# Kernel optimization log

Measured on AMD Instinct MI355X. Metric: run time of the kernel, lower is better.

The kernel has to match this reference:

```python
import jax, jax.numpy as jnp
import numpy as np

N, E, G = 20000, 320000, 64
DIN, H, EF, FC, OUT = 128, 256, 16, 256, 1
BN_EPS = 1e-5


def _gine_layer(x, src, dst, edge_attr, We, be, Wa, ba, g, bt, Wb, bb):
    # GINEConv (eps=0): out = mlp(x + sum_j relu(x_j + lin_edge(e_ij)))
    e = edge_attr @ We.T + be                      # [E, in_ch]
    m = jax.nn.relu(x[src] + e)                    # messages [E, in_ch]
    agg = jax.ops.segment_sum(m, dst, num_segments=x.shape[0])
    h = (x + agg) @ Wa.T + ba                      # Linear
    # BatchNorm1d in eval mode with running_mean=0, running_var=1
    inv = jax.lax.rsqrt(jnp.asarray(1.0 + BN_EPS, h.dtype))
    h = jax.nn.relu(h * inv * g + bt)
    return jax.nn.relu(h @ Wb.T + bb)


def _mean_pool(h, batch, num_graphs):
    sums = jax.ops.segment_sum(h, batch, num_segments=num_graphs)
    cnt = jax.ops.segment_sum(jnp.ones((h.shape[0],), h.dtype), batch, num_segments=num_graphs)
    return sums / jnp.maximum(cnt, 1.0)[:, None]


def setup_inputs() -> dict:
    key = jax.random.key(0)
    ks = iter(jax.random.split(key, 64))

    def nrm(shape, s=0.05):
        return jax.random.normal(next(ks), shape, jnp.float32) * s

    inp = {
        "x": jax.random.normal(next(ks), (N, DIN), jnp.float32),
        "edge_attr": jax.random.normal(next(ks), (E, EF), jnp.float32),
        "src": jax.random.randint(next(ks), (E,), 0, N),
        "dst": jax.random.randint(next(ks), (E,), 0, N),
        "batch": jnp.sort(jax.random.randint(next(ks), (N,), 0, G)),
    }
    dims = [(DIN, H), (H, H), (H, H)]
    for i, (din, h) in enumerate(dims, start=1):
        inp[f"We{i}"] = nrm((din, EF));  inp[f"be{i}"] = jnp.zeros((din,), jnp.float32)
        inp[f"Wa{i}"] = nrm((h, din));  inp[f"ba{i}"] = jnp.zeros((h,), jnp.float32)
        inp[f"g{i}"] = jnp.ones((h,), jnp.float32); inp[f"bt{i}"] = jnp.zeros((h,), jnp.float32)
        inp[f"Wb{i}"] = nrm((h, h));    inp[f"bb{i}"] = jnp.zeros((h,), jnp.float32)
    inp["L1w"] = nrm((FC * 3, H * 3)); inp["L1b"] = jnp.zeros((FC * 3,), jnp.float32)
    inp["L2w"] = nrm((OUT, FC * 3));   inp["L2b"] = jnp.zeros((OUT,), jnp.float32)
    return inp


def reference(x, edge_attr, src, dst, batch,
              We1, be1, Wa1, ba1, g1, bt1, Wb1, bb1,
              We2, be2, Wa2, ba2, g2, bt2, Wb2, bb2,
              We3, be3, Wa3, ba3, g3, bt3, Wb3, bb3,
              L1w, L1b, L2w, L2b):
    h1 = _gine_layer(x,  src, dst, edge_attr, We1, be1, Wa1, ba1, g1, bt1, Wb1, bb1)
    h2 = _gine_layer(h1, src, dst, edge_attr, We2, be2, Wa2, ba2, g2, bt2, Wb2, bb2)
    h3 = _gine_layer(h2, src, dst, edge_attr, We3, be3, Wa3, ba3, g3, bt3, Wb3, bb3)
    p = jnp.concatenate([_mean_pool(h1, batch, G),
                         _mean_pool(h2, batch, G),
                         _mean_pool(h3, batch, G)], axis=1)   # [G, 3H]
    h = jax.nn.relu(p @ L1w.T + L1b)   # dropout is identity (training=False)
    return jax.nn.sigmoid(h @ L2w.T + L2b)
```

## Files before the change

### kernel.cpp

```cpp
#include <hip/hip_runtime.h>
#include <math.h>
#include <stdint.h>

#define N_NODES 20000
#define M_PAD 20032
#define N_EDGES 320000
#define N_GRAPHS 64
#define DIN 128
#define H 256
#define POOL_W 768
#define CHUNK 40
#define NCHUNK (N_EDGES / CHUNK)

typedef __attribute__((ext_vector_type(8))) short bf16x8;
typedef __attribute__((ext_vector_type(4))) float f32x4;
typedef __attribute__((ext_vector_type(4))) unsigned int u32x4;
typedef __attribute__((ext_vector_type(2))) unsigned int u32x2;
typedef _Float16 h2 __attribute__((ext_vector_type(2)));

__device__ __forceinline__ unsigned short f2bf(float f) {
    unsigned u = __builtin_bit_cast(unsigned, f);
    u += 0x7FFFu + ((u >> 16) & 1u);
    return (unsigned short)(u >> 16);
}
__device__ __forceinline__ float bf2f(unsigned short u) {
    return __builtin_bit_cast(float, (unsigned)u << 16);
}
__device__ __forceinline__ unsigned short f2h(float f) {
    const _Float16 h = (_Float16)f;
    return __builtin_bit_cast(unsigned short, h);
}

#if __has_builtin(__builtin_amdgcn_fdot2)
#define DOT2(a, b, c) __builtin_amdgcn_fdot2((a), (b), (c), false)
#else
__device__ __forceinline__ float dot2_fallback(h2 a, h2 b, float c) {
    return fmaf((float)a.x, (float)b.x, fmaf((float)a.y, (float)b.y, c));
}
#define DOT2(a, b, c) dot2_fallback((a), (b), (c))
#endif

struct CvtJob  { const float* s; unsigned short* d; int n4; int mode; int kdim; };
struct CvtJobs { CvtJob j[12]; };

__global__ __launch_bounds__(256) void cvt_all(CvtJobs jobs)
{
    const CvtJob J = jobs.j[blockIdx.y];
    if (J.mode == 2) {
        const ushort4 z = {0, 0, 0, 0};
        for (int i = blockIdx.x * 256 + threadIdx.x; i < J.n4; i += gridDim.x * 256)
            ((ushort4*)J.d)[i] = z;
        return;
    }
    if (J.mode == 1) {
        for (int i = blockIdx.x * 256 + threadIdx.x; i < J.n4; i += gridDim.x * 256) {
            const float4 v = ((const float4*)J.s)[i];
            ushort4 r;
            r.x = f2h(v.x); r.y = f2h(v.y); r.z = f2h(v.z); r.w = f2h(v.w);
            ((ushort4*)J.d)[i] = r;
        }
        return;
    }
    if (J.mode == 3) {
        const int K = J.kdim, KC = K / 32;
        for (int t = blockIdx.x * 256 + threadIdx.x; t < J.n4; t += gridDim.x * 256) {
            int unit = t;
            const int lane = unit & 63; unit >>= 6;
            const int half = unit & 1;  unit >>= 1;
            const int c = unit % KC;
            const int g = unit / KC;
            const int row = g * 32 + half * 16 + (lane & 15);
            const int kb  = c * 32 + ((lane >> 4) << 3);
            const float4 v0 = *(const float4*)(J.s + (size_t)row * K + kb);
            const float4 v1 = *(const float4*)(J.s + (size_t)row * K + kb + 4);
            ushort4 r0, r1;
            r0.x = f2bf(v0.x); r0.y = f2bf(v0.y); r0.z = f2bf(v0.z); r0.w = f2bf(v0.w);
            r1.x = f2bf(v1.x); r1.y = f2bf(v1.y); r1.z = f2bf(v1.z); r1.w = f2bf(v1.w);
            ushort4* dst = (ushort4*)(J.d + (size_t)t * 8);
            dst[0] = r0; dst[1] = r1;
        }
        return;
    }
    for (int i = blockIdx.x * 256 + threadIdx.x; i < J.n4; i += gridDim.x * 256) {
        const float4 v = ((const float4*)J.s)[i];
        ushort4 r;
        r.x = f2bf(v.x); r.y = f2bf(v.y); r.z = f2bf(v.z); r.w = f2bf(v.w);
        ((ushort4*)J.d)[i] = r;
    }
}

__global__ __launch_bounds__(256) void hist_kernel(const int* __restrict__ dst,
                                                   int* __restrict__ deg)
{
    const int i = blockIdx.x * 256 + threadIdx.x;
    if (i < N_EDGES) atomicAdd(deg + dst[i], 1);
}

__global__ __launch_bounds__(1024) void scan_kernel(const int* __restrict__ deg,
                                                    int* __restrict__ off,
                                                    int* __restrict__ cur,
                                                    const int* __restrict__ batch,
                                                    int* __restrict__ start)
{
    __shared__ int wsum[16];
    __shared__ int carry;
    const int tid = threadIdx.x, wave = tid >> 6, lane = tid & 63;
    if (tid == 0) carry = 0;
    __syncthreads();
    for (int base = 0; base < N_NODES; base += 1024) {
        const int i = base + tid;
        const int v = (i < N_NODES) ? deg[i] : 0;
        int s = v;
#pragma unroll
        for (int d = 1; d < 64; d <<= 1) {
            const int t = __shfl_up(s, d);
            if (lane >= d) s += t;
        }
        if (lane == 63) wsum[wave] = s;
        __syncthreads();
        if (wave == 0) {
            int t = (lane < 16) ? wsum[lane] : 0;
#pragma unroll
            for (int d = 1; d < 16; d <<= 1) {
                const int u = __shfl_up(t, d);
                if (lane >= d) t += u;
            }
            if (lane < 16) wsum[lane] = t;
        }
        __syncthreads();
        const int wbase = (wave == 0) ? 0 : wsum[wave - 1];
        if (i < N_NODES) {
            const int o = carry + wbase + s - v;
            off[i] = o;
            cur[i] = o;
        }
        const int tot = wsum[15];
        __syncthreads();
        if (tid == 0) carry += tot;
        __syncthreads();
    }
    if (tid == 0) off[N_NODES] = carry;

    if (tid <= N_GRAPHS) {
        if (tid == N_GRAPHS) { start[N_GRAPHS] = N_NODES; }
        else {
            int lo = 0, hi = N_NODES;
            while (lo < hi) { const int mid = (lo + hi) >> 1; if (batch[mid] < tid) lo = mid + 1; else hi = mid; }
            start[tid] = lo;
        }
    }
}

__global__ __launch_bounds__(256) void chunkmap_kernel(const int* __restrict__ off,
                                                       int* __restrict__ cmap)
{
    const int w = blockIdx.x * 256 + threadIdx.x;
    if (w > NCHUNK) return;
    if (w == NCHUNK) { cmap[w] = N_NODES; return; }
    const int target = w * CHUNK;
    int lo = 0, hi = N_NODES;
    while (lo < hi) { const int mid = (lo + hi) >> 1; if (off[mid] < target) lo = mid + 1; else hi = mid; }
    cmap[w] = lo;
}

__global__ __launch_bounds__(256) void scatter_kernel(
    const int* __restrict__ src, const int* __restrict__ dst,
    const float* __restrict__ ea, int* __restrict__ cursor,
    int* __restrict__ ssrc, unsigned short* __restrict__ eas)
{
    const int e = blockIdx.x * 256 + threadIdx.x;
    if (e < N_EDGES) {
        const int p = atomicAdd(cursor + dst[e], 1);
        ssrc[p] = src[e];
        const float4* er = (const float4*)(ea + (size_t)e * 16);
        unsigned short* dr = eas + (size_t)p * 16;
        ushort4* d4 = (ushort4*)dr;
#pragma unroll
        for (int q = 0; q < 4; ++q) {
            const float4 v = er[q];
            ushort4 r;
            r.x = f2h(v.x); r.y = f2h(v.y); r.z = f2h(v.z); r.w = f2h(v.w);
            d4[q] = r;
        }
    }
}

template<int IN>
__global__ __launch_bounds__(256, 4) void agg3(
    const unsigned short* __restrict__ xb,
    const unsigned short* __restrict__ eas,
    const int* __restrict__ ssrc,
    const int* __restrict__ off,
    const int* __restrict__ cmap,
    const unsigned short* __restrict__ Weh,
    const float* __restrict__ be,
    unsigned short* __restrict__ out)
{
    constexpr int CPL = IN / 64;
    constexpr int XW  = CPL / 2;
    const int lane = threadIdx.x & 63;
    const int wid  = blockIdx.x * 4 + (threadIdx.x >> 6);
    const int c0 = lane * CPL;
    const int zd = __builtin_amdgcn_mbcnt_lo(0u, 0u);

    u32x4 wlo[CPL], whi[CPL];
    float bias[CPL], acc[CPL];
#pragma unroll
    for (int j = 0; j < CPL; ++j) {
        const u32x4* wr = (const u32x4*)(Weh + (size_t)(c0 + j) * 16);
        wlo[j] = wr[0];
        whi[j] = wr[1];
        bias[j] = be[c0 + j];
        acc[j]  = 0.0f;
    }
#pragma unroll
    for (int j = 0; j < CPL; ++j) {
#pragma unroll
        for (int k = 0; k < 4; ++k) {
            { float t = __builtin_bit_cast(float, wlo[j][k]); asm volatile("" : "+v"(t)); wlo[j][k] = __builtin_bit_cast(unsigned int, t); }
            { float t = __builtin_bit_cast(float, whi[j][k]); asm volatile("" : "+v"(t)); whi[j][k] = __builtin_bit_cast(unsigned int, t); }
        }
        asm volatile("" : "+v"(bias[j]));
    }

    int n          = __builtin_amdgcn_readfirstlane(cmap[wid]);
    const int nend = __builtin_amdgcn_readfirstlane(cmap[wid + 1]);
    if (n >= nend) return;
    int p          = __builtin_amdgcn_readfirstlane(off[n]);
    const int pend = __builtin_amdgcn_readfirstlane(off[nend]);

    auto ldx = [&](int s) -> u32x2 {
        if constexpr (XW == 2) {
            return *(const u32x2*)(xb + (size_t)s * IN + c0);
        } else {
            u32x2 r;
            r[0] = *(const unsigned int*)(xb + (size_t)s * IN + c0);
            r[1] = 0u;
            return r;
        }
    };
    auto flushv = [&](int nn, u32x2 xs) {
        if constexpr (XW == 2) {
            const float x0 = __builtin_bit_cast(float, xs[0] << 16);
            const float x1 = __builtin_bit_cast(float, xs[0] & 0xFFFF0000u);
            const float x2 = __builtin_bit_cast(float, xs[1] << 16);
            const float x3 = __builtin_bit_cast(float, xs[1] & 0xFFFF0000u);
            u32x2 o;
            o[0] = (unsigned)f2bf(x0 + acc[0]) | ((unsigned)f2bf(x1 + acc[1]) << 16);
            o[1] = (unsigned)f2bf(x2 + acc[2]) | ((unsigned)f2bf(x3 + acc[3]) << 16);
            *(u32x2*)(out + (size_t)nn * IN + c0) = o;
        } else {
            const float x0 = __builtin_bit_cast(float, xs[0] << 16);
            const float x1 = __builtin_bit_cast(float, xs[0] & 0xFFFF0000u);
            const unsigned int o =
                (unsigned)f2bf(x0 + acc[0]) | ((unsigned)f2bf(x1 + acc[1]) << 16);
            *(unsigned int*)(out + (size_t)nn * IN + c0) = o;
        }
#pragma unroll
        for (int j = 0; j < CPL; ++j) acc[j] = 0.0f;
    };

    int p1 = __builtin_amdgcn_readfirstlane(off[n + 1]);
    while (p1 == p) {
        flushv(n, ldx(n)); ++n;
        if (n >= nend) return;
        p1 = __builtin_amdgcn_readfirstlane(off[n + 1]);
    }
    u32x2 xself = ldx(n);

    auto ldeL = [&](int q) -> u32x4 {
        return ((const u32x4*)(eas + (size_t)(q + zd) * 16))[0];
    };
    auto ldeH = [&](int q) -> u32x4 {
        return ((const u32x4*)(eas + (size_t)(q + zd) * 16))[1];
    };
    auto ldsrc = [&](int q) -> int {
        const int qc = (q < N_EDGES) ? q : (N_EDGES - 1);
        return ssrc[qc + zd];
    };
    auto edge_compute = [&](u32x4 eL, u32x4 eH, u32x2 xw) {
        float m[CPL];
#pragma unroll
        for (int j = 0; j < CPL; ++j) m[j] = bias[j];
#pragma unroll
        for (int k = 0; k < 4; ++k) {
            const h2 ep = __builtin_bit_cast(h2, eL[k]);
#pragma unroll
            for (int j = 0; j < CPL; ++j)
                m[j] = DOT2(ep, __builtin_bit_cast(h2, wlo[j][k]), m[j]);
        }
#pragma unroll
        for (int k = 0; k < 4; ++k) {
            const h2 ep = __builtin_bit_cast(h2, eH[k]);
#pragma unroll
            for (int j = 0; j < CPL; ++j)
                m[j] = DOT2(ep, __builtin_bit_cast(h2, whi[j][k]), m[j]);
        }
#pragma unroll
        for (int j = 0; j < CPL; ++j) {
            const unsigned int word = xw[j >> 1];
            const float xf = __builtin_bit_cast(float,
                (j & 1) ? (word & 0xFFFF0000u) : (word << 16));
            acc[j] += fmaxf(m[j] + xf, 0.0f);
        }
    };
    auto adv = [&]() {
        flushv(n, xself); ++n;
        while (n < nend) {
            p1 = __builtin_amdgcn_readfirstlane(off[n + 1]);
            if (p1 != p) { xself = ldx(n); break; }
            flushv(n, ldx(n)); ++n;
        }
    };

    int sA = ldsrc(p),     sB = ldsrc(p + 1), sC = ldsrc(p + 2), sD = ldsrc(p + 3);
    u32x4 eLA = ldeL(p),     eHA = ldeH(p);
    u32x4 eLB = ldeL(p + 1), eHB = ldeH(p + 1);
    u32x4 eLC = ldeL(p + 2), eHC = ldeH(p + 2);
    u32x4 eLD = ldeL(p + 3), eHD = ldeH(p + 3);
    u32x2 xA = ldx(sA), xB = ldx(sB), xC = ldx(sC), xD = ldx(sD);
    sA = ldsrc(p + 4); sB = ldsrc(p + 5); sC = ldsrc(p + 6); sD = ldsrc(p + 7);

    for (;;) {
        edge_compute(eLA, eHA, xA);
        eLA = ldeL(p + 4); eHA = ldeH(p + 4); xA = ldx(sA); sA = ldsrc(p + 8);
        ++p; if (p == p1) adv();
        if (p >= pend) break;

        edge_compute(eLB, eHB, xB);
        eLB = ldeL(p + 4); eHB = ldeH(p + 4); xB = ldx(sB); sB = ldsrc(p + 8);
        ++p; if (p == p1) adv();
        if (p >= pend) break;

        edge_compute(eLC, eHC, xC);
        eLC = ldeL(p + 4); eHC = ldeH(p + 4); xC = ldx(sC); sC = ldsrc(p + 8);
        ++p; if (p == p1) adv();
        if (p >= pend) break;

        edge_compute(eLD, eHD, xD);
        eLD = ldeL(p + 4); eHD = ldeH(p + 4); xD = ldx(sD); sD = ldsrc(p + 8);
        ++p; if (p == p1) adv();
        if (p >= pend) break;
    }
    while (n < nend) { flushv(n, ldx(n)); ++n; }
}

template<int K>
__global__ __launch_bounds__(512, 4) void gemm_fused(
    const unsigned short* __restrict__ A,
    const unsigned short* __restrict__ WaF,
    const float* __restrict__ ba,
    const float* __restrict__ gsc, const float* __restrict__ bsh,
    const unsigned short* __restrict__ WbF,
    const float* __restrict__ bb,
    unsigned short* __restrict__ out)
{
    constexpr int KC1 = K / 32;
    constexpr int KC2 = H / 32;
    constexpr int SLOTS = K / 8;
    __shared__ unsigned short Al[64 * K];
    __shared__ unsigned short Tl[64 * H];

    const int w = threadIdx.x >> 6, lane = threadIdx.x & 63;
    const int lm = lane & 15, lq = lane >> 4;
    const int n0 = w * 32;
    const int m0 = blockIdx.x * 64;

    const bf16x8* Wa8 = (const bf16x8*)WaF;
    const bf16x8* Wb8 = (const bf16x8*)WbF;

#pragma unroll
    for (int i = 0; i < 64 * SLOTS / 512; ++i) {
        const int t = i * 512 + threadIdx.x;
        const int row = t / SLOTS, slot = t % SLOTS;
        const uint4 v = *(const uint4*)(A + (size_t)(m0 + row) * K + slot * 8);
        *(uint4*)((char*)Al + row * (K * 2) + ((slot ^ (row & 7)) * 16)) = v;
    }

    const float inv = rsqrtf(1.0f + 1e-5f);
    const float bc0 = ba[n0 + lm],  bc1 = ba[n0 + 16 + lm];
    const float gc0 = gsc[n0 + lm], gc1 = gsc[n0 + 16 + lm];
    const float sc0 = bsh[n0 + lm], sc1 = bsh[n0 + 16 + lm];

    __syncthreads();

    {
        f32x4 acc0[4], acc1[4];
#pragma unroll
        for (int ch = 0; ch < 4; ++ch) {
            acc0[ch] = (f32x4){0.f, 0.f, 0.f, 0.f};
            acc1[ch] = (f32x4){0.f, 0.f, 0.f, 0.f};
        }
#pragma unroll
        for (int kh = 0; kh < KC1; kh += 4) {
            bf16x8 C0[4], C1[4];
#pragma unroll
            for (int c = 0; c < 4; ++c) {
                const int fi = (w * KC1 + kh + c) * 2;
                C0[c] = Wa8[(size_t)(fi + 0) * 64 + lane];
                C1[c] = Wa8[(size_t)(fi + 1) * 64 + lane];
            }
#pragma unroll
            for (int ch = 0; ch < 4; ++ch) {
                const int row = ch * 16 + lm;
                const char* rbase = (const char*)Al + row * (K * 2);
#pragma unroll
                for (int c = 0; c < 4; ++c) {
                    const int slot = (lq + (kh + c) * 4) ^ (row & 7);
                    const bf16x8 a = *(const bf16x8*)(rbase + slot * 16);
                    acc0[ch] = __builtin_amdgcn_mfma_f32_16x16x32_bf16(a, C0[c], acc0[ch], 0, 0, 0);
                    acc1[ch] = __builtin_amdgcn_mfma_f32_16x16x32_bf16(a, C1[c], acc1[ch], 0, 0, 0);
                }
            }
        }
#pragma unroll
        for (int ch = 0; ch < 4; ++ch) {
#pragma unroll
            for (int r = 0; r < 4; ++r) {
                const int rowo = ch * 16 + lq * 4 + r;
                const float v0 = fmaxf((acc0[ch][r] + bc0) * inv * gc0 + sc0, 0.0f);
                const float v1 = fmaxf((acc1[ch][r] + bc1) * inv * gc1 + sc1, 0.0f);
                const int col0 = n0 + lm, col1 = n0 + 16 + lm;
                *(unsigned short*)((char*)Tl + rowo * (H * 2)
                    + (((col0 >> 3) ^ (rowo & 7)) << 4) + ((col0 & 7) << 1)) = f2bf(v0);
                *(unsigned short*)((char*)Tl + rowo * (H * 2)
                    + (((col1 >> 3) ^ (rowo & 7)) << 4) + ((col1 & 7) << 1)) = f2bf(v1);
            }
        }
    }

    const float eb0 = bb[n0 + lm], eb1 = bb[n0 + 16 + lm];

    __syncthreads();

    {
        f32x4 acc0[4], acc1[4];
#pragma unroll
        for (int ch = 0; ch < 4; ++ch) {
            acc0[ch] = (f32x4){0.f, 0.f, 0.f, 0.f};
            acc1[ch] = (f32x4){0.f, 0.f, 0.f, 0.f};
        }
#pragma unroll
        for (int kh = 0; kh < KC2; kh += 4) {
            bf16x8 C0[4], C1[4];
#pragma unroll
            for (int c = 0; c < 4; ++c) {
                const int fi = (w * KC2 + kh + c) * 2;
                C0[c] = Wb8[(size_t)(fi + 0) * 64 + lane];
                C1[c] = Wb8[(size_t)(fi + 1) * 64 + lane];
            }
#pragma unroll
            for (int ch = 0; ch < 4; ++ch) {
                const int row = ch * 16 + lm;
                const char* rbase = (const char*)Tl + row * (H * 2);
#pragma unroll
                for (int c = 0; c < 4; ++c) {
                    const int slot = (lq + (kh + c) * 4) ^ (row & 7);
                    const bf16x8 a = *(const bf16x8*)(rbase + slot * 16);
                    acc0[ch] = __builtin_amdgcn_mfma_f32_16x16x32_bf16(a, C0[c], acc0[ch], 0, 0, 0);
                    acc1[ch] = __builtin_amdgcn_mfma_f32_16x16x32_bf16(a, C1[c], acc1[ch], 0, 0, 0);
                }
            }
        }
#pragma unroll
        for (int ch = 0; ch < 4; ++ch) {
            const int mr = m0 + ch * 16;
#pragma unroll
            for (int r = 0; r < 4; ++r) {
                const int rowo = mr + lq * 4 + r;
                if (rowo >= N_NODES) continue;
                const float v0 = fmaxf(acc0[ch][r] + eb0, 0.0f);
                const float v1 = fmaxf(acc1[ch][r] + eb1, 0.0f);
                out[(size_t)rowo * H + n0 + lm]      = f2bf(v0);
                out[(size_t)rowo * H + n0 + 16 + lm] = f2bf(v1);
            }
        }
    }
}

#define RSPLIT 6
__global__ __launch_bounds__(256) void pool2(
    const unsigned short* __restrict__ h1, const unsigned short* __restrict__ h2,
    const unsigned short* __restrict__ h3, const int* __restrict__ start,
    float* __restrict__ pool)
{
    const int g = blockIdx.x & 63, layer = blockIdx.x >> 6;
    const unsigned short* h = (layer == 0) ? h1 : (layer == 1) ? h2 : h3;
    const int r0 = start[g], r1 = start[g + 1];
    const int nr = r1 - r0;
    if (nr <= 0) return;
    const int chunk = (nr + RSPLIT - 1) / RSPLIT;
    const int rs = r0 + blockIdx.y * chunk;
    const int re = (rs + chunk < r1) ? rs + chunk : r1;
    if (rs >= re) return;

    const int c = threadIdx.x;
    float s0 = 0.f, s1 = 0.f, s2 = 0.f, s3 = 0.f;
    int r = rs;
    for (; r + 4 <= re; r += 4) {
        s0 += bf2f(h[(size_t)(r + 0) * H + c]);
        s1 += bf2f(h[(size_t)(r + 1) * H + c]);
        s2 += bf2f(h[(size_t)(r + 2) * H + c]);
        s3 += bf2f(h[(size_t)(r + 3) * H + c]);
    }
    for (; r < re; ++r) s0 += bf2f(h[(size_t)r * H + c]);
    atomicAdd(&pool[(size_t)g * POOL_W + layer * 256 + c], s0 + s1 + s2 + s3);
}

__global__ __launch_bounds__(256) void fc_head(
    const float* __restrict__ pool, const int* __restrict__ start,
    const float* __restrict__ L1w, const float* __restrict__ L1b,
    const float* __restrict__ L2w, float* __restrict__ gsum)
{
    const int g = blockIdx.x;
    __shared__ float p[POOL_W];

    const float rc = 1.0f / fmaxf((float)(start[g + 1] - start[g]), 1.0f);
    for (int i = threadIdx.x; i < POOL_W; i += 256)
        p[i] = pool[(size_t)g * POOL_W + i] * rc;
    __syncthreads();

    const int wv = threadIdx.x >> 6, lane = threadIdx.x & 63;
    const float4* p4 = (const float4*)p;
    const float4 pa = p4[lane], pb = p4[lane + 64], pc = p4[lane + 128];

    const int ob = blockIdx.y * 64 + wv * 16;
    float part = 0.0f;
#pragma unroll 4
    for (int t = 0; t < 16; ++t) {
        const int o = ob + t;
        const float4* wr = (const float4*)(L1w + (size_t)o * POOL_W);
        const float4 a = wr[lane], b = wr[lane + 64], c = wr[lane + 128];
        float acc = a.x * pa.x + a.y * pa.y + a.z * pa.z + a.w * pa.w
                  + b.x * pb.x + b.y * pb.y + b.z * pb.z + b.w * pb.w
                  + c.x * pc.x + c.y * pc.y + c.z * pc.z + c.w * pc.w;
#pragma unroll
        for (int off = 32; off > 0; off >>= 1) acc += __shfl_xor(acc, off);
        if (lane == 0) part += fmaxf(acc + L1b[o], 0.0f) * L2w[o];
    }
    if (lane == 0) atomicAdd(&gsum[g], part);
}

__global__ __launch_bounds__(64) void sig_kernel(
    const float* __restrict__ gsum, const float* __restrict__ L2b,
    float* __restrict__ out)
{
    const int g = threadIdx.x;
    if (g < N_GRAPHS) out[g] = 1.0f / (1.0f + expf(-(gsum[g] + L2b[0])));
}

extern "C" void kernel_launch(void* const* d_in, const int* in_sizes, int n_in,
                              void* d_out, int out_size, void* d_ws, size_t ws_size,
                              hipStream_t stream)
{
    const float* x     = (const float*)d_in[0];
    const float* ea    = (const float*)d_in[1];
    const int*   src   = (const int*)d_in[2];
    const int*   dst   = (const int*)d_in[3];
    const int*   batch = (const int*)d_in[4];

    const float* We[3]; const float* be[3]; const float* Wa[3]; const float* ba[3];
    const float* gg[3]; const float* bt[3]; const float* Wb[3]; const float* bb[3];
    for (int l = 0; l < 3; ++l) {
        const int o = 5 + 8 * l;
        We[l] = (const float*)d_in[o + 0]; be[l] = (const float*)d_in[o + 1];
        Wa[l] = (const float*)d_in[o + 2]; ba[l] = (const float*)d_in[o + 3];
        gg[l] = (const float*)d_in[o + 4]; bt[l] = (const float*)d_in[o + 5];
        Wb[l] = (const float*)d_in[o + 6]; bb[l] = (const float*)d_in[o + 7];
    }
    const float* L1w = (const float*)d_in[29];
    const float* L1b = (const float*)d_in[30];
    const float* L2w = (const float*)d_in[31];
    const float* L2b = (const float*)d_in[32];

    float* pool   = (float*)d_ws;
    float* gsum   = pool + (size_t)N_GRAPHS * POOL_W;
    int*   deg    = (int*)(gsum + N_GRAPHS);
    int*   off    = deg + N_NODES;
    int*   cursor = off + N_NODES + 1;
    int*   start  = cursor + N_NODES;
    int*   cmap   = start + 72;
    int*   ssrc   = (int*)((((uintptr_t)(cmap + NCHUNK + 1)) + 31) & ~(uintptr_t)31);
    unsigned short* eas = (unsigned short*)((((uintptr_t)(ssrc + N_EDGES + 16)) + 31) & ~(uintptr_t)31);
    unsigned short* xb = (unsigned short*)((((uintptr_t)(eas + (size_t)(N_EDGES + 16) * 16)) + 31) & ~(uintptr_t)31);
    unsigned short* u  = xb + (size_t)M_PAD * DIN;
    unsigned short* h1 = u  + (size_t)M_PAD * H;
    unsigned short* h2 = h1 + (size_t)M_PAD * H;
    unsigned short* h3 = h2 + (size_t)M_PAD * H;
    unsigned short* wbf[6];
    wbf[0] = h3 + (size_t)M_PAD * H;
    wbf[1] = wbf[0] + H * DIN;
    for (int i = 2; i < 6; ++i) wbf[i] = wbf[i - 1] + H * H;
    unsigned short* weh[3];
    weh[0] = wbf[5] + H * H;
    weh[1] = weh[0] + DIN * 16;
    weh[2] = weh[1] + H * 16;

    CvtJobs jobs;
    jobs.j[0]  = { x,       xb,                    N_NODES * DIN / 4,       0, 0 };
    jobs.j[1]  = { Wa[0],   wbf[0],                H * DIN / 8,             3, DIN };
    jobs.j[2]  = { Wb[0],   wbf[1],                H * H / 8,               3, H };
    jobs.j[3]  = { Wa[1],   wbf[2],                H * H / 8,               3, H };
    jobs.j[4]  = { Wb[1],   wbf[3],                H * H / 8,               3, H };
    jobs.j[5]  = { Wa[2],   wbf[4],                H * H / 8,               3, H };
    jobs.j[6]  = { Wb[2],   wbf[5],                H * H / 8,               3, H };
    jobs.j[7]  = { nullptr, (unsigned short*)deg,  N_NODES * 4 / 8,         2, 0 };
    jobs.j[8]  = { nullptr, (unsigned short*)pool, (N_GRAPHS * POOL_W + N_GRAPHS) * 4 / 8, 2, 0 };
    jobs.j[9]  = { We[0],   weh[0],                DIN * 16 / 4,            1, 0 };
    jobs.j[10] = { We[1],   weh[1],                H * 16 / 4,              1, 0 };
    jobs.j[11] = { We[2],   weh[2],                H * 16 / 4,              1, 0 };
    cvt_all<<<dim3(320, 12), 256, 0, stream>>>(jobs);

    hist_kernel<<<(N_EDGES + 255) / 256, 256, 0, stream>>>(dst, deg);
    scan_kernel<<<1, 1024, 0, stream>>>(deg, off, cursor, batch, start);
    chunkmap_kernel<<<(NCHUNK + 256) / 256, 256, 0, stream>>>(off, cmap);
    scatter_kernel<<<(N_EDGES + 255) / 256, 256, 0, stream>>>(src, dst, ea, cursor, ssrc, eas);

    const int agrid = NCHUNK / 4;
    const int ggrid = M_PAD / 64;

    agg3<DIN><<<agrid, 256, 0, stream>>>(xb, eas, ssrc, off, cmap, weh[0], be[0], u);
    gemm_fused<DIN><<<ggrid, 512, 0, stream>>>(u, wbf[0], ba[0], gg[0], bt[0], wbf[1], bb[0], h1);
    agg3<H><<<agrid, 256, 0, stream>>>(h1, eas, ssrc, off, cmap, weh[1], be[1], u);
    gemm_fused<H><<<ggrid, 512, 0, stream>>>(u, wbf[2], ba[1], gg[1], bt[1], wbf[3], bb[1], h2);
    agg3<H><<<agrid, 256, 0, stream>>>(h2, eas, ssrc, off, cmap, weh[2], be[2], u);
    gemm_fused<H><<<ggrid, 512, 0, stream>>>(u, wbf[4], ba[2], gg[2], bt[2], wbf[5], bb[2], h3);

    pool2<<<dim3(3 * N_GRAPHS, RSPLIT), 256, 0, stream>>>(h1, h2, h3, start, pool);
    fc_head<<<dim3(N_GRAPHS, POOL_W / 64), 256, 0, stream>>>(pool, start, L1w, L1b, L2w, gsum);
    sig_kernel<<<1, 64, 0, stream>>>(gsum, L2b, (float*)d_out);
}
```

Measured before the change: 455.4 us.

## Fold chunkmap into scatter, vectorize pool loads, process two graphs per fc_head block

The chunk-map binary search now runs in extra blocks appended to the scatter kernel, so one launch disappears. The pooling kernel reads 16-byte vectors of eight bf16 values per thread across eight row groups and reduces them in shared memory, instead of making scalar 2-byte loads. fc_head handles two graphs per block so each L1w row is read once for both graphs, halving weight traffic. These are small tail kernels, so the overall effect is likely minor.

```diff
diff --git a/kernel.cpp b/kernel.cpp
--- a/kernel.cpp
+++ b/kernel.cpp
@@ -11,6 +11,8 @@
 #define POOL_W 768
 #define CHUNK 40
 #define NCHUNK (N_EDGES / CHUNK)
+#define EDGE_BLOCKS ((N_EDGES + 255) / 256)
+#define CMAP_BLOCKS ((NCHUNK + 1 + 255) / 256)
 
 typedef __attribute__((ext_vector_type(8))) short bf16x8;
 typedef __attribute__((ext_vector_type(4))) float f32x4;
@@ -151,30 +153,28 @@
     }
 }
 
-__global__ __launch_bounds__(256) void chunkmap_kernel(const int* __restrict__ off,
-                                                       int* __restrict__ cmap)
-{
-    const int w = blockIdx.x * 256 + threadIdx.x;
-    if (w > NCHUNK) return;
-    if (w == NCHUNK) { cmap[w] = N_NODES; return; }
-    const int target = w * CHUNK;
-    int lo = 0, hi = N_NODES;
-    while (lo < hi) { const int mid = (lo + hi) >> 1; if (off[mid] < target) lo = mid + 1; else hi = mid; }
-    cmap[w] = lo;
-}
-
 __global__ __launch_bounds__(256) void scatter_kernel(
     const int* __restrict__ src, const int* __restrict__ dst,
     const float* __restrict__ ea, int* __restrict__ cursor,
-    int* __restrict__ ssrc, unsigned short* __restrict__ eas)
-{
+    int* __restrict__ ssrc, unsigned short* __restrict__ eas,
+    const int* __restrict__ off, int* __restrict__ cmap)
+{
+    if (blockIdx.x >= EDGE_BLOCKS) {
+        const int w = (blockIdx.x - EDGE_BLOCKS) * 256 + threadIdx.x;
+        if (w > NCHUNK) return;
+        if (w == NCHUNK) { cmap[w] = N_NODES; return; }
+        const int target = w * CHUNK;
+        int lo = 0, hi = N_NODES;
+        while (lo < hi) { const int mid = (lo + hi) >> 1; if (off[mid] < target) lo = mid + 1; else hi = mid; }
+        cmap[w] = lo;
+        return;
+    }
     const int e = blockIdx.x * 256 + threadIdx.x;
     if (e < N_EDGES) {
         const int p = atomicAdd(cursor + dst[e], 1);
         ssrc[p] = src[e];
         const float4* er = (const float4*)(ea + (size_t)e * 16);
-        unsigned short* dr = eas + (size_t)p * 16;
-        ushort4* d4 = (ushort4*)dr;
+        ushort4* d4 = (ushort4*)(eas + (size_t)p * 16);
 #pragma unroll
         for (int q = 0; q < 4; ++q) {
             const float4 v = er[q];
@@ -494,17 +494,31 @@
     const int re = (rs + chunk < r1) ? rs + chunk : r1;
     if (rs >= re) return;
 
-    const int c = threadIdx.x;
+    const int cg = threadIdx.x & 31;
+    const int rg = threadIdx.x >> 5;
     float s0 = 0.f, s1 = 0.f, s2 = 0.f, s3 = 0.f;
-    int r = rs;
-    for (; r + 4 <= re; r += 4) {
-        s0 += bf2f(h[(size_t)(r + 0) * H + c]);
-        s1 += bf2f(h[(size_t)(r + 1) * H + c]);
-        s2 += bf2f(h[(size_t)(r + 2) * H + c]);
-        s3 += bf2f(h[(size_t)(r + 3) * H + c]);
-    }
-    for (; r < re; ++r) s0 += bf2f(h[(size_t)r * H + c]);
-    atomicAdd(&pool[(size_t)g * POOL_W + layer * 256 + c], s0 + s1 + s2 + s3);
+    float s4 = 0.f, s5 = 0.f, s6 = 0.f, s7 = 0.f;
+    for (int r = rs + rg; r < re; r += 8) {
+        const u32x4 v = *(const u32x4*)(h + (size_t)r * H + cg * 8);
+        s0 += __builtin_bit_cast(float, v[0] << 16);
+        s1 += __builtin_bit_cast(float, v[0] & 0xFFFF0000u);
+        s2 += __builtin_bit_cast(float, v[1] << 16);
+        s3 += __builtin_bit_cast(float, v[1] & 0xFFFF0000u);
+        s4 += __builtin_bit_cast(float, v[2] << 16);
+        s5 += __builtin_bit_cast(float, v[2] & 0xFFFF0000u);
+        s6 += __builtin_bit_cast(float, v[3] << 16);
+        s7 += __builtin_bit_cast(float, v[3] & 0xFFFF0000u);
+    }
+    __shared__ float red[8][256];
+    red[rg][cg * 8 + 0] = s0; red[rg][cg * 8 + 1] = s1;
+    red[rg][cg * 8 + 2] = s2; red[rg][cg * 8 + 3] = s3;
+    red[rg][cg * 8 + 4] = s4; red[rg][cg * 8 + 5] = s5;
+    red[rg][cg * 8 + 6] = s6; red[rg][cg * 8 + 7] = s7;
+    __syncthreads();
+    float t = 0.f;
+#pragma unroll
+    for (int q = 0; q < 8; ++q) t += red[q][threadIdx.x];
+    atomicAdd(&pool[(size_t)g * POOL_W + layer * 256 + threadIdx.x], t);
 }
 
 __global__ __launch_bounds__(256) void fc_head(
@@ -512,33 +526,52 @@
     const float* __restrict__ L1w, const float* __restrict__ L1b,
     const float* __restrict__ L2w, float* __restrict__ gsum)
 {
-    const int g = blockIdx.x;
-    __shared__ float p[POOL_W];
-
-    const float rc = 1.0f / fmaxf((float)(start[g + 1] - start[g]), 1.0f);
-    for (int i = threadIdx.x; i < POOL_W; i += 256)
-        p[i] = pool[(size_t)g * POOL_W + i] * rc;
+    const int g0 = blockIdx.x * 2, g1 = g0 + 1;
+    __shared__ float p[2][POOL_W];
+
+    const float rc0 = 1.0f / fmaxf((float)(start[g0 + 1] - start[g0]), 1.0f);
+    const float rc1 = 1.0f / fmaxf((float)(start[g1 + 1] - start[g1]), 1.0f);
+    for (int i = threadIdx.x; i < POOL_W; i += 256) {
+        p[0][i] = pool[(size_t)g0 * POOL_W + i] * rc0;
+        p[1][i] = pool[(size_t)g1 * POOL_W + i] * rc1;
+    }
     __syncthreads();
 
     const int wv = threadIdx.x >> 6, lane = threadIdx.x & 63;
-    const float4* p4 = (const float4*)p;
-    const float4 pa = p4[lane], pb = p4[lane + 64], pc = p4[lane + 128];
+    const float4* pA = (const float4*)p[0];
+    const float4* pB = (const float4*)p[1];
+    const float4 a0 = pA[lane], a1 = pA[lane + 64], a2 = pA[lane + 128];
+    const float4 b0 = pB[lane], b1 = pB[lane + 64], b2 = pB[lane + 128];
 
     const int ob = blockIdx.y * 64 + wv * 16;
-    float part = 0.0f;
+    float part0 = 0.0f, part1 = 0.0f;
 #pragma unroll 4
     for (int t = 0; t < 16; ++t) {
         const int o = ob + t;
         const float4* wr = (const float4*)(L1w + (size_t)o * POOL_W);
-        const float4 a = wr[lane], b = wr[lane + 64], c = wr[lane + 128];
-        float acc = a.x * pa.x + a.y * pa.y + a.z * pa.z + a.w * pa.w
-                  + b.x * pb.x + b.y * pb.y + b.z * pb.z + b.w * pb.w
-                  + c.x * pc.x + c.y * pc.y + c.z * pc.z + c.w * pc.w;
-#pragma unroll
-        for (int off = 32; off > 0; off >>= 1) acc += __shfl_xor(acc, off);
-        if (lane == 0) part += fmaxf(acc + L1b[o], 0.0f) * L2w[o];
-    }
-    if (lane == 0) atomicAdd(&gsum[g], part);
+        const float4 wa = wr[lane], wb = wr[lane + 64], wc = wr[lane + 128];
+        float accA = wa.x * a0.x + wa.y * a0.y + wa.z * a0.z + wa.w * a0.w
+                   + wb.x * a1.x + wb.y * a1.y + wb.z * a1.z + wb.w * a1.w
+                   + wc.x * a2.x + wc.y * a2.y + wc.z * a2.z + wc.w * a2.w;
+        float accB = wa.x * b0.x + wa.y * b0.y + wa.z * b0.z + wa.w * b0.w
+                   + wb.x * b1.x + wb.y * b1.y + wb.z * b1.z + wb.w * b1.w
+                   + wc.x * b2.x + wc.y * b2.y + wc.z * b2.z + wc.w * b2.w;
+#pragma unroll
+        for (int off = 32; off > 0; off >>= 1) {
+            accA += __shfl_xor(accA, off);
+            accB += __shfl_xor(accB, off);
+        }
+        if (lane == 0) {
+            const float r = fmaxf(accA + L1b[o], 0.0f);
+            const float s = fmaxf(accB + L1b[o], 0.0f);
+            part0 += r * L2w[o];
+            part1 += s * L2w[o];
+        }
+    }
+    if (lane == 0) {
+        atomicAdd(&gsum[g0], part0);
+        atomicAdd(&gsum[g1], part1);
+    }
 }
 
 __global__ __launch_bounds__(64) void sig_kernel(
@@ -611,10 +644,10 @@
     jobs.j[11] = { We[2],   weh[2],                H * 16 / 4,              1, 0 };
     cvt_all<<<dim3(320, 12), 256, 0, stream>>>(jobs);
 
-    hist_kernel<<<(N_EDGES + 255) / 256, 256, 0, stream>>>(dst, deg);
+    hist_kernel<<<EDGE_BLOCKS, 256, 0, stream>>>(dst, deg);
     scan_kernel<<<1, 1024, 0, stream>>>(deg, off, cursor, batch, start);
-    chunkmap_kernel<<<(NCHUNK + 256) / 256, 256, 0, stream>>>(off, cmap);
-    scatter_kernel<<<(N_EDGES + 255) / 256, 256, 0, stream>>>(src, dst, ea, cursor, ssrc, eas);
+    scatter_kernel<<<EDGE_BLOCKS + CMAP_BLOCKS, 256, 0, stream>>>(
+        src, dst, ea, cursor, ssrc, eas, off, cmap);
 
     const int agrid = NCHUNK / 4;
     const int ggrid = M_PAD / 64;
@@ -627,6 +660,6 @@
     gemm_fused<H><<<ggrid, 512, 0, stream>>>(u, wbf[4], ba[2], gg[2], bt[2], wbf[5], bb[2], h3);
 
     pool2<<<dim3(3 * N_GRAPHS, RSPLIT), 256, 0, stream>>>(h1, h2, h3, start, pool);
-    fc_head<<<dim3(N_GRAPHS, POOL_W / 64), 256, 0, stream>>>(pool, start, L1w, L1b, L2w, gsum);
+    fc_head<<<dim3(N_GRAPHS / 2, POOL_W / 64), 256, 0, stream>>>(pool, start, L1w, L1b, L2w, gsum);
     sig_kernel<<<1, 64, 0, stream>>>(gsum, L2b, (float*)d_out);
 }
```

Result: faster. 440.9 us (median of 2 runs) (-3.2%).
